# Kernel tuning notes

Measured on AMD Instinct MI355X. Metric: run time of the kernel, lower is better.

The kernel has to match this reference:

```python
import math
import jax, jax.numpy as jnp
import numpy as np

B, N, E, R = 1024, 200, 256, 256

def _layernorm(x, g, b, eps=1e-5):
    mu = x.mean(-1, keepdims=True)
    var = ((x - mu) ** 2).mean(-1, keepdims=True)
    return (x - mu) / jnp.sqrt(var + eps) * g + b

def setup_inputs() -> dict:
    key = jax.random.key(0)
    ks = jax.random.split(key, 16)
    d = {}
    d["e_emb"] = jax.random.normal(ks[0], (B, E), jnp.float32)
    d["nb_rel"] = jax.random.normal(ks[1], (B, N, R), jnp.float32)
    d["delta_t"] = jax.random.uniform(ks[2], (B, N), jnp.float32) * 10.0
    d["r_emb"] = jax.random.normal(ks[3], (B, R), jnp.float32)
    d["hist_mask"] = jax.random.randint(ks[4], (B, N), 0, 2).astype(bool)
    d["rel_w"] = jax.random.normal(ks[5], (E, R), jnp.float32) / math.sqrt(R)
    d["log_tau1"] = jnp.asarray(1.0, jnp.float32)
    d["log_tau2"] = jnp.asarray(2.5, jnp.float32)
    d["sharpness"] = jnp.asarray(1.5, jnp.float32)
    d["log_gamma"] = jnp.asarray(-2.0, jnp.float32)
    d["attn_w"] = jax.random.normal(ks[6], (3, E, E), jnp.float32) / math.sqrt(E)
    d["sp_w"] = jax.random.normal(ks[7], (3, E, 6 * E), jnp.float32) / math.sqrt(6 * E)
    d["sp_b"] = jnp.zeros((3, E), jnp.float32)
    d["ln_g"] = jnp.ones((3, E), jnp.float32)
    d["ln_b"] = jnp.zeros((3, E), jnp.float32)
    d["csq_w"] = jax.random.normal(ks[8], (E, R), jnp.float32) / math.sqrt(R)
    d["csq_b"] = jnp.zeros((E,), jnp.float32)
    d["csl_w"] = jax.random.normal(ks[9], (3, E), jnp.float32) / math.sqrt(E)
    d["csl_b"] = jnp.zeros((3,), jnp.float32)
    d["on_g"] = jnp.ones((E,), jnp.float32)
    d["on_b"] = jnp.zeros((E,), jnp.float32)
    return d

def _pna_one_scale(msgs, mask, e_emb, q_key, attn_w, sp_w, sp_b, ln_g, ln_b):
    # msgs: [B,N,E], mask: [B,N] bool, e_emb: [B,E], q_key: [B,E]
    valid_f = mask[..., None].astype(msgs.dtype)
    n_valid = jnp.maximum(mask.astype(msgs.dtype).sum(1, keepdims=True), 1.0)  # [B,1]
    msgs_v = msgs * valid_f
    mean_v = msgs_v.sum(1) / n_valid
    max_v = msgs_v.max(1)
    min_v = jnp.clip(jnp.where(mask[..., None], msgs, 10000.0).min(1), -10000.0, 10000.0)
    sq_m = (jnp.clip(msgs_v, -10.0, 10.0) ** 2).sum(1) / n_valid
    std_v = jnp.sqrt(jnp.maximum(sq_m - mean_v ** 2, 1e-6))
    q_proj = q_key @ attn_w.T  # [B,E]
    attn_raw = jnp.einsum('bne,be->bn', msgs, q_proj) / math.sqrt(msgs.shape[-1])
    attn_raw = jnp.where(mask, attn_raw, -10000.0)
    all_invalid = ~mask.any(1, keepdims=True)  # [B,1]
    attn_raw = jnp.where(all_invalid, 0.0, attn_raw)
    attn_p = jax.nn.softmax(attn_raw, axis=-1)
    attn_v = jnp.einsum('bn,bne->be', attn_p, msgs)
    feats = jnp.concatenate([mean_v, max_v, min_v, std_v, attn_v, e_emb], axis=-1)  # [B,6E]
    h = feats @ sp_w.T + sp_b
    h = _layernorm(h, ln_g, ln_b)
    return jax.nn.gelu(h, approximate=False)  # dropout = identity (eval mode)

def reference(e_emb, nb_rel, delta_t, r_emb, hist_mask, rel_w, log_tau1, log_tau2,
              sharpness, log_gamma, attn_w, sp_w, sp_b, ln_g, ln_b,
              csq_w, csq_b, csl_w, csl_b, on_g, on_b):
    msgs = jnp.einsum('bnr,er->bne', nb_rel, rel_w)
    gamma = jnp.exp(log_gamma)
    decay = jnp.exp(-gamma * jnp.maximum(delta_t, 0.0))
    msgs_dec = msgs * decay[..., None]
    tau1 = jnp.exp(log_tau1)
    tau2 = jnp.exp(log_tau2) + tau1
    sharp = jnp.clip(sharpness, 0.1, 5.0)
    w_fine = jax.nn.sigmoid(-sharp * (delta_t - tau1))
    w_coarse = jax.nn.sigmoid(sharp * (delta_t - tau2))
    w_mid = jnp.maximum(1.0 - w_fine - w_coarse, 0.0)
    scale_w = jnp.stack([w_fine, w_mid, w_coarse])  # [3,B,N]
    m_scales = msgs_dec[None] * scale_w[..., None]  # [3,B,N,E]
    q_key = r_emb @ rel_w.T  # [B,E]
    pna_v = jax.vmap(_pna_one_scale, in_axes=(0, None, None, None, 0, 0, 0, 0, 0))
    scales = pna_v(m_scales, hist_mask, e_emb, q_key, attn_w, sp_w, sp_b, ln_g, ln_b)  # [3,B,E]
    sq = r_emb @ csq_w.T + csq_b  # [B,E]
    logits = sq @ csl_w.T + csl_b  # [B,3]
    weights = jax.nn.softmax(logits, axis=-1)
    out = jnp.einsum('bs,sbe->be', weights, scales)
    return _layernorm(out, on_g, on_b)  # drop = identity (eval)
```

## Files before the change

kernel.cpp:

```cpp
#include <hip/hip_runtime.h>
#include <hip/hip_bf16.h>
#include <math.h>

#define B_   1024
#define N_   200
#define NR_  208
#define NT_  13
#define E_   256
#define R_   256
#define K6_  1536

typedef __attribute__((ext_vector_type(8))) short bf16x8;
typedef __attribute__((ext_vector_type(4))) float f32x4;

__device__ __forceinline__ unsigned short f2bf(float f) {
  unsigned int u = __float_as_uint(f);
  u += 0x7fffu + ((u >> 16) & 1u);
  return (unsigned short)(u >> 16);
}

__device__ __forceinline__ unsigned int pk_bf(float lo, float hi) {
  float2 t; t.x = lo; t.y = hi;
  __hip_bfloat162 h = __float22bfloat162_rn(t);
  unsigned int u;
  __builtin_memcpy(&u, &h, 4);
  return u;
}

__device__ __forceinline__ float gelu_exact(float x) {
  return 0.5f * x * (1.f + erff(x * 0.70710678118654752f));
}

__global__ __launch_bounds__(256) void k_cast(const float* __restrict__ rel_w,
                                              const float* __restrict__ sp_w,
                                              unsigned short* __restrict__ rw_bf,
                                              unsigned short* __restrict__ spw_bf) {
  int idx = blockIdx.x * 256 + threadIdx.x;
  if (idx < E_ * R_) rw_bf[idx] = f2bf(rel_w[idx]);
  int j = idx - E_ * R_;
  if (j >= 0 && j < 3 * E_ * K6_) spw_bf[j] = f2bf(sp_w[j]);
}

__global__ __launch_bounds__(256) void k_prep(
    const float* __restrict__ r_emb, const float* __restrict__ rel_w,
    const float* __restrict__ csq_w, const float* __restrict__ csq_b,
    const float* __restrict__ csl_w, const float* __restrict__ csl_b,
    const float* __restrict__ attn_w,
    unsigned short* __restrict__ t_bf, float* __restrict__ wts) {
  __shared__ __align__(16) float re[4][256];
  __shared__ __align__(16) float qk[4][256];
  __shared__ __align__(16) float sqs[4][256];
  __shared__ __align__(16) float qp[3][4][256];
  __shared__ float lg[4][3];
  int b0 = blockIdx.x * 4;
  int tid = threadIdx.x;
  int e = tid;
#pragma unroll
  for (int i = 0; i < 4; ++i)
    re[i][tid] = r_emb[(size_t)(b0 + i) * 256 + tid];
  __syncthreads();
  {
    float qkv[4], sv[4];
#pragma unroll
    for (int i = 0; i < 4; ++i) { qkv[i] = 0.f; sv[i] = 0.f; }
    const float4* w4 = (const float4*)(rel_w) + (size_t)e * 64;
    const float4* c4 = (const float4*)(csq_w) + (size_t)e * 64;
    for (int r = 0; r < 64; ++r) {
      float4 w = w4[r];
      float4 c = c4[r];
#pragma unroll
      for (int i = 0; i < 4; ++i) {
        float4 x = ((const float4*)re[i])[r];
        qkv[i] += w.x * x.x + w.y * x.y + w.z * x.z + w.w * x.w;
        sv[i] += c.x * x.x + c.y * x.y + c.z * x.z + c.w * x.w;
      }
    }
    float cb = csq_b[e];
#pragma unroll
    for (int i = 0; i < 4; ++i) {
      qk[i][e] = qkv[i];
      sqs[i][e] = sv[i] + cb;
    }
  }
  __syncthreads();
  if (tid < 12) {
    int i = tid / 3, k = tid % 3;
    float acc = csl_b[k];
    for (int ee = 0; ee < 256; ++ee) acc += sqs[i][ee] * csl_w[k * 256 + ee];
    lg[i][k] = acc;
  }
  __syncthreads();
  if (tid < 4) {
    float l0 = lg[tid][0], l1 = lg[tid][1], l2 = lg[tid][2];
    float m = fmaxf(l0, fmaxf(l1, l2));
    float e0 = expf(l0 - m), e1 = expf(l1 - m), e2 = expf(l2 - m);
    float inv = 1.f / (e0 + e1 + e2);
    wts[(b0 + tid) * 4 + 0] = e0 * inv;
    wts[(b0 + tid) * 4 + 1] = e1 * inv;
    wts[(b0 + tid) * 4 + 2] = e2 * inv;
  }
  {
    float qpv[3][4];
#pragma unroll
    for (int s = 0; s < 3; ++s)
#pragma unroll
      for (int i = 0; i < 4; ++i) qpv[s][i] = 0.f;
#pragma unroll
    for (int s = 0; s < 3; ++s) {
      const float4* a4 = (const float4*)(attn_w) + ((size_t)s * 256 + e) * 64;
      for (int r = 0; r < 64; ++r) {
        float4 w = a4[r];
#pragma unroll
        for (int i = 0; i < 4; ++i) {
          float4 x = ((const float4*)qk[i])[r];
          qpv[s][i] += w.x * x.x + w.y * x.y + w.z * x.z + w.w * x.w;
        }
      }
    }
    __syncthreads();
#pragma unroll
    for (int s = 0; s < 3; ++s)
#pragma unroll
      for (int i = 0; i < 4; ++i) qp[s][i][e] = qpv[s][i];
  }
  __syncthreads();
  {
    int r = tid;
    float tacc[3][4];
#pragma unroll
    for (int s = 0; s < 3; ++s)
#pragma unroll
      for (int i = 0; i < 4; ++i) tacc[s][i] = 0.f;
    for (int e4 = 0; e4 < 64; ++e4) {
      float4 qv[3][4];
#pragma unroll
      for (int s = 0; s < 3; ++s)
#pragma unroll
        for (int i = 0; i < 4; ++i)
          qv[s][i] = ((const float4*)qp[s][i])[e4];
#pragma unroll
      for (int j = 0; j < 4; ++j) {
        float w = rel_w[(size_t)(e4 * 4 + j) * 256 + r];
#pragma unroll
        for (int s = 0; s < 3; ++s)
#pragma unroll
          for (int i = 0; i < 4; ++i) {
            float q = (j == 0) ? qv[s][i].x : (j == 1) ? qv[s][i].y
                      : (j == 2) ? qv[s][i].z : qv[s][i].w;
            tacc[s][i] = fmaf(q, w, tacc[s][i]);
          }
      }
    }
#pragma unroll
    for (int s = 0; s < 3; ++s)
#pragma unroll
      for (int i = 0; i < 4; ++i)
        t_bf[((size_t)(b0 + i) * 3 + s) * 256 + r] = f2bf(tacc[s][i]);
  }
}

__global__ __launch_bounds__(1024, 4) void k1_main(
    const float* __restrict__ nb_rel, const float* __restrict__ delta_t,
    const unsigned char* __restrict__ hm_raw, const float* __restrict__ e_emb,
    const float* __restrict__ p_lt1, const float* __restrict__ p_lt2,
    const float* __restrict__ p_sh, const float* __restrict__ p_lgm,
    const unsigned short* __restrict__ rw_bf, const unsigned short* __restrict__ t_bf,
    unsigned short* __restrict__ feats) {
  __shared__ __align__(16) struct {
    unsigned int a[2 * 16 * 132];
    float c[3][NR_];
    float p[3][NR_];
    float nmeta[NR_ * 12];
  } sm;
  int b = blockIdx.x;
  int tid = threadIdx.x;
  int lane = tid & 63, wave = tid >> 6;
  int row16 = lane & 15, quad = lane >> 4;

  int hasNZoff = 0, hasFP = 0;
  {
    unsigned char cc = hm_raw[tid];
    if ((tid & 3) != 0 && cc != 0) {
      hasNZoff = 1;
      if (cc == 0x3Fu || cc == 0x80u) hasFP = 1;
    }
  }
  int cntNZ = __syncthreads_count(hasNZoff);
  int cntFP = __syncthreads_count(hasFP);
  int mmode = (cntNZ == 0) ? 0 : (cntFP > 0 ? 2 : 1);

  float tau1 = __expf(p_lt1[0]);
  float tau2 = __expf(p_lt2[0]) + tau1;
  float sharp = fminf(fmaxf(p_sh[0], 0.1f), 5.0f);
  float gamma = __expf(p_lgm[0]);

  bool mk = false;
  if (tid < NR_) {
    float mf = 0.f, c0 = 0.f, c1 = 0.f, c2 = 0.f;
    if (tid < N_) {
      size_t mi = (size_t)b * N_ + tid;
      if (mmode == 0)      mk = ((const int*)hm_raw)[mi] != 0;
      else if (mmode == 1) mk = hm_raw[mi] != 0;
      else                 mk = ((const float*)hm_raw)[mi] != 0.f;
      float dt = delta_t[mi];
      mf = mk ? 1.f : 0.f;
      float decay = __expf(-gamma * fmaxf(dt, 0.f));
      float wf = 1.f / (1.f + __expf(sharp * (dt - tau1)));
      float wc = 1.f / (1.f + __expf(-sharp * (dt - tau2)));
      float wm = fmaxf(1.f - wf - wc, 0.f);
      c0 = decay * wf; c1 = decay * wm; c2 = decay * wc;
    }
    sm.c[0][tid] = c0; sm.c[1][tid] = c1; sm.c[2][tid] = c2;
    f32x4 w0, w1;
    w0[0] = mf * c0; w0[1] = mf * c1; w0[2] = mf * c2; w0[3] = mk ? 0.f : 1e4f;
    w1[0] = 0.f; w1[1] = 0.f; w1[2] = 0.f; w1[3] = mf;
    *(f32x4*)&sm.nmeta[tid * 12]     = w0;
    *(f32x4*)&sm.nmeta[tid * 12 + 4] = w1;
  }
  int cnt = __syncthreads_count(mk ? 1 : 0);
  float nvf = fmaxf((float)cnt, 1.f);
  bool allinv = (cnt == 0);

  const float* srcw = nb_rel + (size_t)b * N_ * 256 + lane * 4;

  bf16x8 tfrag[8];
  {
    int sr = (row16 < 3) ? row16 : 0;
    const unsigned short* tb = t_bf + ((size_t)b * 3 + sr) * 256 + quad * 8;
    bf16x8 zer = {0, 0, 0, 0, 0, 0, 0, 0};
#pragma unroll
    for (int ks = 0; ks < 8; ++ks) {
      bf16x8 tv = *(const bf16x8*)(tb + ks * 32);
      tfrag[ks] = (row16 < 3) ? tv : zer;
    }
  }

  if (wave == 15) {
    for (int i = lane; i < 256; i += 64) {
      unsigned short v = f2bf(e_emb[(size_t)b * 256 + i]);
      feats[((size_t)0 * B_ + b) * K6_ + 1280 + i] = v;
      feats[((size_t)1 * B_ + b) * K6_ + 1280 + i] = v;
      feats[((size_t)2 * B_ + b) * K6_ + 1280 + i] = v;
    }
  }

  {
    float4 x = *(const float4*)(srcw + (size_t)wave * 256);
    uint2 pk;
    pk.x = pk_bf(x.x, x.y);
    pk.y = pk_bf(x.z, x.w);
    *(uint2*)&sm.a[wave * 132 + lane * 2] = pk;
  }
  __syncthreads();

  for (int t = 0; t < NT_; ++t) {
    float4 xn;
    if (t < NT_ - 1) {
      int n = (t + 1) * 16 + wave;
      int gn = (n < N_) ? n : (N_ - 1);
      xn = *(const float4*)(srcw + (size_t)gn * 256);
    }
    if (wave == t) {
      f32x4 acc;
      acc[0] = 0.f; acc[1] = 0.f; acc[2] = 0.f; acc[3] = 0.f;
      const unsigned int* sa = &sm.a[(t & 1) * 2112];
#pragma unroll
      for (int ks = 0; ks < 8; ++ks) {
        bf16x8 af = *(const bf16x8*)&sa[row16 * 132 + ks * 16 + quad * 4];
        acc = __builtin_amdgcn_mfma_f32_16x16x32_bf16(af, tfrag[ks], acc, 0, 0, 0);
      }
      if (row16 < 3) {
#pragma unroll
        for (int rg = 0; rg < 4; ++rg) {
          int n = t * 16 + quad * 4 + rg;
          float cw = sm.c[row16][n];
          float mf = sm.nmeta[n * 12 + 7];
          float l = cw * acc[rg] * 0.0625f;
          l = (mf > 0.5f) ? l : -1e4f;
          if (allinv) l = (n < N_) ? 0.f : -1e4f;
          sm.p[row16][n] = l;
        }
      }
    }
    if (t < NT_ - 1) {
      uint2 pk;
      pk.x = pk_bf(xn.x, xn.y);
      pk.y = pk_bf(xn.z, xn.w);
      *(uint2*)&sm.a[((t + 1) & 1) * 2112 + wave * 132 + lane * 2] = pk;
    }
    __syncthreads();
  }

  bf16x8 bfr[8];
  {
    int e = wave * 16 + row16;
#pragma unroll
    for (int ks = 0; ks < 8; ++ks)
      bfr[ks] = *(const bf16x8*)(rw_bf + (size_t)e * 256 + ks * 32 + quad * 8);
  }
  {
    float4 x = *(const float4*)(srcw + (size_t)wave * 256);
    uint2 pk;
    pk.x = pk_bf(x.x, x.y);
    pk.y = pk_bf(x.z, x.w);
    *(uint2*)&sm.a[wave * 132 + lane * 2] = pk;
  }
  if (wave < 3) {
    int s = wave;
    float m = -1e30f;
    for (int n = lane; n < NR_; n += 64) m = fmaxf(m, sm.p[s][n]);
#pragma unroll
    for (int o = 32; o >= 1; o >>= 1) m = fmaxf(m, __shfl_xor(m, o, 64));
    float ssum = 0.f;
    for (int n = lane; n < NR_; n += 64) {
      float ev = __expf(sm.p[s][n] - m);
      sm.p[s][n] = ev;
      ssum += ev;
    }
#pragma unroll
    for (int o = 32; o >= 1; o >>= 1) ssum += __shfl_xor(ssum, o, 64);
    float inv = 1.f / ssum;
    for (int n = lane; n < NR_; n += 64)
      sm.nmeta[n * 12 + 4 + s] = sm.p[s][n] * inv * sm.c[s][n];
  }
  __syncthreads();

  float s_mean[3], s_mx[3], s_mn[3], s_sq[3], s_av[3];
#pragma unroll
  for (int s = 0; s < 3; ++s) {
    s_mean[s] = 0.f; s_mx[s] = -1e30f; s_mn[s] = 1e30f;
    s_sq[s] = 0.f; s_av[s] = 0.f;
  }

  for (int t = 0; t < NT_; ++t) {
    float4 xn;
    if (t < NT_ - 1) {
      int n = (t + 1) * 16 + wave;
      int gn = (n < N_) ? n : (N_ - 1);
      xn = *(const float4*)(srcw + (size_t)gn * 256);
    }
    f32x4 acc;
    acc[0] = 0.f; acc[1] = 0.f; acc[2] = 0.f; acc[3] = 0.f;
    const unsigned int* sa = &sm.a[(t & 1) * 2112];
#pragma unroll
    for (int ks = 0; ks < 8; ++ks) {
      bf16x8 af = *(const bf16x8*)&sa[row16 * 132 + ks * 16 + quad * 4];
      acc = __builtin_amdgcn_mfma_f32_16x16x32_bf16(af, bfr[ks], acc, 0, 0, 0);
    }
    int nb = t * 16 + quad * 4;
#pragma unroll
    for (int rg = 0; rg < 4; ++rg) {
      const float* nm = &sm.nmeta[(size_t)(nb + rg) * 12];
      f32x4 w0 = *(const f32x4*)nm;
      f32x4 w1 = *(const f32x4*)(nm + 4);
      float m = acc[rg];
#pragma unroll
      for (int s = 0; s < 3; ++s) {
        float vm = w0[s] * m;
        s_mean[s] += vm;
        s_mx[s] = fmaxf(s_mx[s], vm);
        s_mn[s] = fminf(s_mn[s], fmaf(w0[s], m, w0[3]));
        float cv = fminf(fmaxf(vm, -10.f), 10.f);
        s_sq[s] = fmaf(cv, cv, s_sq[s]);
        s_av[s] = fmaf(w1[s], m, s_av[s]);
      }
    }
    if (t < NT_ - 1) {
      uint2 pk;
      pk.x = pk_bf(xn.x, xn.y);
      pk.y = pk_bf(xn.z, xn.w);
      *(uint2*)&sm.a[((t + 1) & 1) * 2112 + wave * 132 + lane * 2] = pk;
    }
    __syncthreads();
  }

#pragma unroll
  for (int s = 0; s < 3; ++s) {
    float vmean = s_mean[s];
    vmean += __shfl_xor(vmean, 16, 64); vmean += __shfl_xor(vmean, 32, 64);
    float vmx = s_mx[s];
    vmx = fmaxf(vmx, __shfl_xor(vmx, 16, 64)); vmx = fmaxf(vmx, __shfl_xor(vmx, 32, 64));
    float vmn = s_mn[s];
    vmn = fminf(vmn, __shfl_xor(vmn, 16, 64)); vmn = fminf(vmn, __shfl_xor(vmn, 32, 64));
    float vsq = s_sq[s];
    vsq += __shfl_xor(vsq, 16, 64); vsq += __shfl_xor(vsq, 32, 64);
    float vav = s_av[s];
    vav += __shfl_xor(vav, 16, 64); vav += __shfl_xor(vav, 32, 64);
    if (lane < 16) {
      int e = wave * 16 + lane;
      size_t base = ((size_t)s * B_ + b) * K6_;
      float meanv = vmean / nvf;
      float stdv = sqrtf(fmaxf(vsq / nvf - meanv * meanv, 1e-6f));
      float mnv = fminf(fmaxf(vmn, -1e4f), 1e4f);
      feats[base + e] = f2bf(meanv);
      feats[base + 256 + e] = f2bf(vmx);
      feats[base + 512 + e] = f2bf(mnv);
      feats[base + 768 + e] = f2bf(stdv);
      feats[base + 1024 + e] = f2bf(vav);
    }
  }
}

__global__ __launch_bounds__(256) void k2_kernel(
    const unsigned short* __restrict__ feats, const unsigned short* __restrict__ spw_bf,
    const float* __restrict__ sp_b, float* __restrict__ hbuf) {
  __shared__ __align__(16) unsigned int a[16 * 132];
  int id = blockIdx.x;
  int s = id >> 7;
  int rem = id & 127;
  int b0 = (rem >> 1) * 16;
  int e0 = (rem & 1) * 128;
  int tid = threadIdx.x, lane = tid & 63, wave = tid >> 6;
  int row16 = lane & 15, quad = lane >> 4;
  f32x4 acc[2];
#pragma unroll
  for (int t = 0; t < 2; ++t)
#pragma unroll
    for (int cc = 0; cc < 4; ++cc) acc[t][cc] = 0.f;

  for (int kc = 0; kc < 6; ++kc) {
    __syncthreads();
    for (int j = tid; j < 512; j += 256) {
      int rw = j >> 5, ck = j & 31;
      bf16x8 v = *(const bf16x8*)(feats + ((size_t)s * B_ + b0 + rw) * K6_ + kc * 256 + ck * 8);
      *(bf16x8*)((unsigned short*)&a[rw * 132] + ck * 8) = v;
    }
    __syncthreads();
#pragma unroll
    for (int ks = 0; ks < 8; ++ks) {
      bf16x8 af = *(const bf16x8*)&a[row16 * 132 + ks * 16 + quad * 4];
#pragma unroll
      for (int t = 0; t < 2; ++t) {
        int e = e0 + wave * 32 + t * 16 + row16;
        bf16x8 bfr = *(const bf16x8*)(spw_bf + ((size_t)s * E_ + e) * K6_ + kc * 256 + ks * 32 + quad * 8);
        acc[t] = __builtin_amdgcn_mfma_f32_16x16x32_bf16(af, bfr, acc[t], 0, 0, 0);
      }
    }
  }
#pragma unroll
  for (int t = 0; t < 2; ++t) {
    int e = e0 + wave * 32 + t * 16 + row16;
    float bias = sp_b[s * 256 + e];
#pragma unroll
    for (int rg = 0; rg < 4; ++rg) {
      int rw = quad * 4 + rg;
      hbuf[((size_t)s * B_ + b0 + rw) * 256 + e] = acc[t][rg] + bias;
    }
  }
}

__global__ __launch_bounds__(256) void k3_kernel(
    const float* __restrict__ hbuf, const float* __restrict__ wts,
    const float* __restrict__ ln_g, const float* __restrict__ ln_b,
    const float* __restrict__ on_g, const float* __restrict__ on_b,
    float* __restrict__ out) {
  __shared__ float rs[4], rq[4];
  int b = blockIdx.x, tid = threadIdx.x, lane = tid & 63, wave = tid >> 6;
  float o = 0.f;
#pragma unroll
  for (int s = 0; s < 3; ++s) {
    float h = hbuf[((size_t)s * B_ + b) * 256 + tid];
    float sum = h, sq = h * h;
#pragma unroll
    for (int off = 32; off >= 1; off >>= 1) {
      sum += __shfl_xor(sum, off, 64);
      sq += __shfl_xor(sq, off, 64);
    }
    if (lane == 0) { rs[wave] = sum; rq[wave] = sq; }
    __syncthreads();
    float ts = rs[0] + rs[1] + rs[2] + rs[3];
    float tq = rq[0] + rq[1] + rq[2] + rq[3];
    __syncthreads();
    float mu = ts * (1.f / 256.f);
    float var = tq * (1.f / 256.f) - mu * mu;
    float rstd = rsqrtf(var + 1e-5f);
    float v = (h - mu) * rstd * ln_g[s * 256 + tid] + ln_b[s * 256 + tid];
    o += wts[b * 4 + s] * gelu_exact(v);
  }
  float sum = o, sq = o * o;
#pragma unroll
  for (int off = 32; off >= 1; off >>= 1) {
    sum += __shfl_xor(sum, off, 64);
    sq += __shfl_xor(sq, off, 64);
  }
  if (lane == 0) { rs[wave] = sum; rq[wave] = sq; }
  __syncthreads();
  float ts = rs[0] + rs[1] + rs[2] + rs[3];
  float tq = rq[0] + rq[1] + rq[2] + rq[3];
  float mu = ts * (1.f / 256.f);
  float var = tq * (1.f / 256.f) - mu * mu;
  float rstd = rsqrtf(var + 1e-5f);
  out[(size_t)b * 256 + tid] = (o - mu) * rstd * on_g[tid] + on_b[tid];
}

extern "C" void kernel_launch(void* const* d_in, const int* in_sizes, int n_in,
                              void* d_out, int out_size, void* d_ws, size_t ws_size,
                              hipStream_t stream) {
  const float* e_emb   = (const float*)d_in[0];
  const float* nb_rel  = (const float*)d_in[1];
  const float* delta_t = (const float*)d_in[2];
  const float* r_emb   = (const float*)d_in[3];
  const unsigned char* hist_mask = (const unsigned char*)d_in[4];
  const float* rel_w   = (const float*)d_in[5];
  const float* lt1     = (const float*)d_in[6];
  const float* lt2     = (const float*)d_in[7];
  const float* shp     = (const float*)d_in[8];
  const float* lgm     = (const float*)d_in[9];
  const float* attn_w  = (const float*)d_in[10];
  const float* sp_w    = (const float*)d_in[11];
  const float* sp_b    = (const float*)d_in[12];
  const float* ln_g    = (const float*)d_in[13];
  const float* ln_b    = (const float*)d_in[14];
  const float* csq_w   = (const float*)d_in[15];
  const float* csq_b   = (const float*)d_in[16];
  const float* csl_w   = (const float*)d_in[17];
  const float* csl_b   = (const float*)d_in[18];
  const float* on_g    = (const float*)d_in[19];
  const float* on_b    = (const float*)d_in[20];
  float* out = (float*)d_out;

  char* ws = (char*)d_ws;
  unsigned short* rw_bf  = (unsigned short*)(ws + 0);
  unsigned short* spw_bf = (unsigned short*)(ws + 131072);
  unsigned short* t_bf   = (unsigned short*)(ws + 2490368);
  float* wts    = (float*)(ws + 4063232);
  unsigned short* feats = (unsigned short*)(ws + 4079616);
  float* hbuf   = (float*)(ws + 13516800);

  hipLaunchKernelGGL(k_cast, dim3(4864), dim3(256), 0, stream, rel_w, sp_w, rw_bf, spw_bf);
  hipLaunchKernelGGL(k_prep, dim3(256), dim3(256), 0, stream, r_emb, rel_w, csq_w, csq_b,
                     csl_w, csl_b, attn_w, t_bf, wts);
  hipLaunchKernelGGL(k1_main, dim3(1024), dim3(1024), 0, stream, nb_rel, delta_t, hist_mask,
                     e_emb, lt1, lt2, shp, lgm, rw_bf, t_bf, feats);
  hipLaunchKernelGGL(k2_kernel, dim3(384), dim3(256), 0, stream, feats, spw_bf, sp_b, hbuf);
  hipLaunchKernelGGL(k3_kernel, dim3(1024), dim3(256), 0, stream, hbuf, wts, ln_g, ln_b,
                     on_g, on_b, out);
}
```

Baseline: 542.7 us.

## Fuse attention-logit and message passes with online softmax, split k2 finer

Before, k1_main made two passes over nb_rel: one to compute attention logits and the softmax, and one to compute the message statistics. It now makes one pass, computing both MFMAs per tile and keeping a running-max (online) softmax with rescaled weighted sum and denominator, normalising at the end. The decay-scale coefficients move into the nmeta shared array, removing separate shared buffers. k2 now uses 768 blocks with 64 output columns each to raise parallelism. The cost is more exp and shuffle work per tile in every wave, since previously only one wave computed logits for each tile.

Result: slower. 674.7 us (+24.3%).

```diff
diff --git a/kernel.cpp b/kernel.cpp
--- a/kernel.cpp
+++ b/kernel.cpp
@@ -168,8 +168,6 @@
     unsigned short* __restrict__ feats) {
   __shared__ __align__(16) struct {
     unsigned int a[2 * 16 * 132];
-    float c[3][NR_];
-    float p[3][NR_];
     float nmeta[NR_ * 12];
   } sm;
   int b = blockIdx.x;
@@ -210,10 +208,9 @@
       float wm = fmaxf(1.f - wf - wc, 0.f);
       c0 = decay * wf; c1 = decay * wm; c2 = decay * wc;
     }
-    sm.c[0][tid] = c0; sm.c[1][tid] = c1; sm.c[2][tid] = c2;
     f32x4 w0, w1;
     w0[0] = mf * c0; w0[1] = mf * c1; w0[2] = mf * c2; w0[3] = mk ? 0.f : 1e4f;
-    w1[0] = 0.f; w1[1] = 0.f; w1[2] = 0.f; w1[3] = mf;
+    w1[0] = c0; w1[1] = c1; w1[2] = c2; w1[3] = mf;
     *(f32x4*)&sm.nmeta[tid * 12]     = w0;
     *(f32x4*)&sm.nmeta[tid * 12 + 4] = w1;
   }
@@ -234,14 +231,19 @@
       tfrag[ks] = (row16 < 3) ? tv : zer;
     }
   }
-
-  if (wave == 15) {
-    for (int i = lane; i < 256; i += 64) {
-      unsigned short v = f2bf(e_emb[(size_t)b * 256 + i]);
-      feats[((size_t)0 * B_ + b) * K6_ + 1280 + i] = v;
-      feats[((size_t)1 * B_ + b) * K6_ + 1280 + i] = v;
-      feats[((size_t)2 * B_ + b) * K6_ + 1280 + i] = v;
-    }
+  bf16x8 bfr[8];
+  {
+    int e = wave * 16 + row16;
+#pragma unroll
+    for (int ks = 0; ks < 8; ++ks)
+      bfr[ks] = *(const bf16x8*)(rw_bf + (size_t)e * 256 + ks * 32 + quad * 8);
+  }
+
+  if (tid < 256) {
+    unsigned short v = f2bf(e_emb[(size_t)b * 256 + tid]);
+    feats[((size_t)0 * B_ + b) * K6_ + 1280 + tid] = v;
+    feats[((size_t)1 * B_ + b) * K6_ + 1280 + tid] = v;
+    feats[((size_t)2 * B_ + b) * K6_ + 1280 + tid] = v;
   }
 
   {
@@ -252,6 +254,17 @@
     *(uint2*)&sm.a[wave * 132 + lane * 2] = pk;
   }
   __syncthreads();
+
+  float m_run[3] = {-1e30f, -1e30f, -1e30f};
+  float s_mean[3], s_mx[3], s_mn[3], s_sq[3], s_av[3], s_ss[3];
+#pragma unroll
+  for (int s = 0; s < 3; ++s) {
+    s_mean[s] = 0.f; s_mx[s] = -1e30f; s_mn[s] = 1e30f;
+    s_sq[s] = 0.f; s_av[s] = 0.f; s_ss[s] = 0.f;
+  }
+
+  int sr = (row16 < 3) ? row16 : 0;
+  int srcb = quad << 4;
 
   for (int t = 0; t < NT_; ++t) {
     float4 xn;
@@ -260,109 +273,70 @@
       int gn = (n < N_) ? n : (N_ - 1);
       xn = *(const float4*)(srcw + (size_t)gn * 256);
     }
-    if (wave == t) {
-      f32x4 acc;
-      acc[0] = 0.f; acc[1] = 0.f; acc[2] = 0.f; acc[3] = 0.f;
-      const unsigned int* sa = &sm.a[(t & 1) * 2112];
-#pragma unroll
-      for (int ks = 0; ks < 8; ++ks) {
-        bf16x8 af = *(const bf16x8*)&sa[row16 * 132 + ks * 16 + quad * 4];
-        acc = __builtin_amdgcn_mfma_f32_16x16x32_bf16(af, tfrag[ks], acc, 0, 0, 0);
-      }
-      if (row16 < 3) {
-#pragma unroll
-        for (int rg = 0; rg < 4; ++rg) {
-          int n = t * 16 + quad * 4 + rg;
-          float cw = sm.c[row16][n];
-          float mf = sm.nmeta[n * 12 + 7];
-          float l = cw * acc[rg] * 0.0625f;
-          l = (mf > 0.5f) ? l : -1e4f;
-          if (allinv) l = (n < N_) ? 0.f : -1e4f;
-          sm.p[row16][n] = l;
-        }
-      }
-    }
-    if (t < NT_ - 1) {
-      uint2 pk;
-      pk.x = pk_bf(xn.x, xn.y);
-      pk.y = pk_bf(xn.z, xn.w);
-      *(uint2*)&sm.a[((t + 1) & 1) * 2112 + wave * 132 + lane * 2] = pk;
-    }
-    __syncthreads();
-  }
-
-  bf16x8 bfr[8];
-  {
-    int e = wave * 16 + row16;
-#pragma unroll
-    for (int ks = 0; ks < 8; ++ks)
-      bfr[ks] = *(const bf16x8*)(rw_bf + (size_t)e * 256 + ks * 32 + quad * 8);
-  }
-  {
-    float4 x = *(const float4*)(srcw + (size_t)wave * 256);
-    uint2 pk;
-    pk.x = pk_bf(x.x, x.y);
-    pk.y = pk_bf(x.z, x.w);
-    *(uint2*)&sm.a[wave * 132 + lane * 2] = pk;
-  }
-  if (wave < 3) {
-    int s = wave;
-    float m = -1e30f;
-    for (int n = lane; n < NR_; n += 64) m = fmaxf(m, sm.p[s][n]);
-#pragma unroll
-    for (int o = 32; o >= 1; o >>= 1) m = fmaxf(m, __shfl_xor(m, o, 64));
-    float ssum = 0.f;
-    for (int n = lane; n < NR_; n += 64) {
-      float ev = __expf(sm.p[s][n] - m);
-      sm.p[s][n] = ev;
-      ssum += ev;
-    }
-#pragma unroll
-    for (int o = 32; o >= 1; o >>= 1) ssum += __shfl_xor(ssum, o, 64);
-    float inv = 1.f / ssum;
-    for (int n = lane; n < NR_; n += 64)
-      sm.nmeta[n * 12 + 4 + s] = sm.p[s][n] * inv * sm.c[s][n];
-  }
-  __syncthreads();
-
-  float s_mean[3], s_mx[3], s_mn[3], s_sq[3], s_av[3];
-#pragma unroll
-  for (int s = 0; s < 3; ++s) {
-    s_mean[s] = 0.f; s_mx[s] = -1e30f; s_mn[s] = 1e30f;
-    s_sq[s] = 0.f; s_av[s] = 0.f;
-  }
-
-  for (int t = 0; t < NT_; ++t) {
-    float4 xn;
-    if (t < NT_ - 1) {
-      int n = (t + 1) * 16 + wave;
-      int gn = (n < N_) ? n : (N_ - 1);
-      xn = *(const float4*)(srcw + (size_t)gn * 256);
-    }
-    f32x4 acc;
-    acc[0] = 0.f; acc[1] = 0.f; acc[2] = 0.f; acc[3] = 0.f;
     const unsigned int* sa = &sm.a[(t & 1) * 2112];
+    f32x4 am, al;
+    am[0] = 0.f; am[1] = 0.f; am[2] = 0.f; am[3] = 0.f;
+    al[0] = 0.f; al[1] = 0.f; al[2] = 0.f; al[3] = 0.f;
 #pragma unroll
     for (int ks = 0; ks < 8; ++ks) {
       bf16x8 af = *(const bf16x8*)&sa[row16 * 132 + ks * 16 + quad * 4];
-      acc = __builtin_amdgcn_mfma_f32_16x16x32_bf16(af, bfr[ks], acc, 0, 0, 0);
-    }
-    int nb = t * 16 + quad * 4;
+      am = __builtin_amdgcn_mfma_f32_16x16x32_bf16(af, bfr[ks], am, 0, 0, 0);
+      al = __builtin_amdgcn_mfma_f32_16x16x32_bf16(af, tfrag[ks], al, 0, 0, 0);
+    }
+    int rowbase = t * 16 + quad * 4;
+    float l[4];
 #pragma unroll
     for (int rg = 0; rg < 4; ++rg) {
-      const float* nm = &sm.nmeta[(size_t)(nb + rg) * 12];
-      f32x4 w0 = *(const f32x4*)nm;
-      f32x4 w1 = *(const f32x4*)(nm + 4);
-      float m = acc[rg];
+      int row = rowbase + rg;
+      float cw  = sm.nmeta[row * 12 + 4 + sr];
+      float mfv = sm.nmeta[row * 12 + 7];
+      float lv = cw * al[rg] * 0.0625f;
+      lv = (mfv > 0.5f) ? lv : -1e4f;
+      if (allinv) lv = (row < N_) ? 0.f : -1e4f;
+      l[rg] = lv;
+    }
+    float tm = fmaxf(fmaxf(l[0], l[1]), fmaxf(l[2], l[3]));
+    tm = fmaxf(tm, __shfl_xor(tm, 16, 64));
+    tm = fmaxf(tm, __shfl_xor(tm, 32, 64));
+    float nmv0 = __shfl(tm, 0, 64);
+    float nmv1 = __shfl(tm, 1, 64);
+    float nmv2 = __shfl(tm, 2, 64);
+    float f[3];
+    {
+      float nmv[3] = {nmv0, nmv1, nmv2};
 #pragma unroll
       for (int s = 0; s < 3; ++s) {
-        float vm = w0[s] * m;
+        float nn = fmaxf(m_run[s], nmv[s]);
+        f[s] = __expf(m_run[s] - nn);
+        m_run[s] = nn;
+        s_av[s] *= f[s];
+        s_ss[s] *= f[s];
+      }
+    }
+    float nmown = (row16 == 0) ? m_run[0] : ((row16 == 1) ? m_run[1] : m_run[2]);
+    float p[4];
+#pragma unroll
+    for (int rg = 0; rg < 4; ++rg) p[rg] = __expf(l[rg] - nmown);
+#pragma unroll
+    for (int rg = 0; rg < 4; ++rg) {
+      float p0 = __shfl(p[rg], srcb + 0, 64);
+      float p1 = __shfl(p[rg], srcb + 1, 64);
+      float p2 = __shfl(p[rg], srcb + 2, 64);
+      const float* nmp = &sm.nmeta[(size_t)(rowbase + rg) * 12];
+      f32x4 w0 = *(const f32x4*)nmp;
+      f32x4 w1 = *(const f32x4*)(nmp + 4);
+      float mm = am[rg];
+      float pv[3] = {p0, p1, p2};
+#pragma unroll
+      for (int s = 0; s < 3; ++s) {
+        float vm = w0[s] * mm;
         s_mean[s] += vm;
         s_mx[s] = fmaxf(s_mx[s], vm);
-        s_mn[s] = fminf(s_mn[s], fmaf(w0[s], m, w0[3]));
+        s_mn[s] = fminf(s_mn[s], fmaf(w0[s], mm, w0[3]));
         float cv = fminf(fmaxf(vm, -10.f), 10.f);
         s_sq[s] = fmaf(cv, cv, s_sq[s]);
-        s_av[s] = fmaf(w1[s], m, s_av[s]);
+        s_av[s] = fmaf(pv[s] * w1[s], mm, s_av[s]);
+        s_ss[s] += pv[s];
       }
     }
     if (t < NT_ - 1) {
@@ -386,6 +360,8 @@
     vsq += __shfl_xor(vsq, 16, 64); vsq += __shfl_xor(vsq, 32, 64);
     float vav = s_av[s];
     vav += __shfl_xor(vav, 16, 64); vav += __shfl_xor(vav, 32, 64);
+    float vss = s_ss[s];
+    vss += __shfl_xor(vss, 16, 64); vss += __shfl_xor(vss, 32, 64);
     if (lane < 16) {
       int e = wave * 16 + lane;
       size_t base = ((size_t)s * B_ + b) * K6_;
@@ -396,7 +372,7 @@
       feats[base + 256 + e] = f2bf(vmx);
       feats[base + 512 + e] = f2bf(mnv);
       feats[base + 768 + e] = f2bf(stdv);
-      feats[base + 1024 + e] = f2bf(vav);
+      feats[base + 1024 + e] = f2bf(vav / vss);
     }
   }
 }
@@ -406,17 +382,16 @@
     const float* __restrict__ sp_b, float* __restrict__ hbuf) {
   __shared__ __align__(16) unsigned int a[16 * 132];
   int id = blockIdx.x;
-  int s = id >> 7;
-  int rem = id & 127;
-  int b0 = (rem >> 1) * 16;
-  int e0 = (rem & 1) * 128;
+  int s = id >> 8;
+  int rem = id & 255;
+  int b0 = (rem >> 2) * 16;
+  int e0 = (rem & 3) * 64;
   int tid = threadIdx.x, lane = tid & 63, wave = tid >> 6;
   int row16 = lane & 15, quad = lane >> 4;
-  f32x4 acc[2];
-#pragma unroll
-  for (int t = 0; t < 2; ++t)
-#pragma unroll
-    for (int cc = 0; cc < 4; ++cc) acc[t][cc] = 0.f;
+  int e = e0 + wave * 16 + row16;
+  f32x4 acc;
+#pragma unroll
+  for (int cc = 0; cc < 4; ++cc) acc[cc] = 0.f;
 
   for (int kc = 0; kc < 6; ++kc) {
     __syncthreads();
@@ -429,22 +404,16 @@
 #pragma unroll
     for (int ks = 0; ks < 8; ++ks) {
       bf16x8 af = *(const bf16x8*)&a[row16 * 132 + ks * 16 + quad * 4];
-#pragma unroll
-      for (int t = 0; t < 2; ++t) {
-        int e = e0 + wave * 32 + t * 16 + row16;
-        bf16x8 bfr = *(const bf16x8*)(spw_bf + ((size_t)s * E_ + e) * K6_ + kc * 256 + ks * 32 + quad * 8);
-        acc[t] = __builtin_amdgcn_mfma_f32_16x16x32_bf16(af, bfr, acc[t], 0, 0, 0);
-      }
-    }
-  }
-#pragma unroll
-  for (int t = 0; t < 2; ++t) {
-    int e = e0 + wave * 32 + t * 16 + row16;
+      bf16x8 bfr = *(const bf16x8*)(spw_bf + ((size_t)s * E_ + e) * K6_ + kc * 256 + ks * 32 + quad * 8);
+      acc = __builtin_amdgcn_mfma_f32_16x16x32_bf16(af, bfr, acc, 0, 0, 0);
+    }
+  }
+  {
     float bias = sp_b[s * 256 + e];
 #pragma unroll
     for (int rg = 0; rg < 4; ++rg) {
       int rw = quad * 4 + rg;
-      hbuf[((size_t)s * B_ + b0 + rw) * 256 + e] = acc[t][rg] + bias;
+      hbuf[((size_t)s * B_ + b0 + rw) * 256 + e] = acc[rg] + bias;
     }
   }
 }
@@ -532,7 +501,7 @@
                      csl_w, csl_b, attn_w, t_bf, wts);
   hipLaunchKernelGGL(k1_main, dim3(1024), dim3(1024), 0, stream, nb_rel, delta_t, hist_mask,
                      e_emb, lt1, lt2, shp, lgm, rw_bf, t_bf, feats);
-  hipLaunchKernelGGL(k2_kernel, dim3(384), dim3(256), 0, stream, feats, spw_bf, sp_b, hbuf);
+  hipLaunchKernelGGL(k2_kernel, dim3(768), dim3(256), 0, stream, feats, spw_bf, sp_b, hbuf);
   hipLaunchKernelGGL(k3_kernel, dim3(1024), dim3(256), 0, stream, hbuf, wts, ln_g, ln_b,
                      on_g, on_b, out);
 }
```
